# Kernel optimization log

Measured on AMD Instinct MI355X. Metric: run time of the kernel, lower is better.

The kernel has to match this reference:

```python
import jax, jax.numpy as jnp
import numpy as np

D_V, D_Q, D_H = 256, 128, 64

def setup_inputs() -> dict:
    key = jax.random.key(0)
    ks = jax.random.split(key, 8)
    B, T = 512, 512
    query = jax.random.normal(ks[0], (B, D_Q), dtype=jnp.float32)
    values = jax.random.normal(ks[1], (B, T, D_V), dtype=jnp.float32)
    s1 = 1.0 / np.sqrt(D_V)
    s2 = 1.0 / np.sqrt(D_Q)
    sv = 1.0 / np.sqrt(D_H)
    W1 = jax.random.uniform(ks[2], (D_H, D_V), jnp.float32, -s1, s1)
    b1 = jax.random.uniform(ks[3], (D_H,), jnp.float32, -s1, s1)
    W2 = jax.random.uniform(ks[4], (D_H, D_Q), jnp.float32, -s2, s2)
    b2 = jax.random.uniform(ks[5], (D_H,), jnp.float32, -s2, s2)
    Wv = jax.random.uniform(ks[6], (1, D_H), jnp.float32, -sv, sv)
    bv = jax.random.uniform(ks[7], (1,), jnp.float32, -sv, sv)
    return {"query": query, "values": values, "W1": W1, "b1": b1,
            "W2": W2, "b2": b2, "Wv": Wv, "bv": bv}

def reference(query, values, W1, b1, W2, b2, Wv, bv):
    # hidden_with_time_axis: [B,1,128]
    h = jnp.einsum('btv,hv->bth', values, W1) + b1 \
        + (jnp.einsum('bq,hq->bh', query, W2) + b2)[:, None, :]   # [B,T,64]
    score = jnp.einsum('bth,oh->bto', jnp.tanh(h), Wv) + bv        # [B,T,1]
    attention_weights = jax.nn.softmax(score, axis=0)              # softmax over dim 0, as written
    context_vector = jnp.sum(attention_weights * values, axis=0)   # [T,256]
    return (context_vector, attention_weights)
```

## Files before the change

kernel.cpp:

```cpp
#include <hip/hip_runtime.h>
#include <hip/hip_bf16.h>

#define Tt 512
#define Bb 512
#define DV 256
#define DQ 128
#define DH 64
#define CTXN (Tt * DV)
#define VBF_BYTES ((size_t)Bb * Tt * DV * 2)

typedef __attribute__((ext_vector_type(8))) short bf16x8;
typedef __attribute__((ext_vector_type(8))) unsigned short u16x8;
typedef __attribute__((ext_vector_type(4))) float f32x4;

__device__ __forceinline__ unsigned short f2bf(float x) {
  unsigned u = __float_as_uint(x);
  u += 0x7FFFu + ((u >> 16) & 1u);
  return (unsigned short)(u >> 16);
}
__device__ __forceinline__ float bf2f(unsigned short b) {
  return __uint_as_float(((unsigned)b) << 16);
}

__global__ void prep_kernel(const float* __restrict__ query,
                            const float* __restrict__ W1,
                            const float* __restrict__ W2,
                            const float* __restrict__ b1,
                            const float* __restrict__ b2,
                            float* __restrict__ qh,
                            unsigned short* __restrict__ w1bf) {
  __shared__ float q[DQ];
  const int blk = blockIdx.x;
  const int h = threadIdx.x;
  if (blk < Bb) {
    q[h]      = query[blk * DQ + h];
    q[h + 64] = query[blk * DQ + h + 64];
    __syncthreads();
    const float* w2r = W2 + h * DQ;
    float acc = 0.f;
#pragma unroll 8
    for (int k = 0; k < DQ; ++k) acc = fmaf(w2r[k], q[k], acc);
    qh[blk * DH + h] = acc + b1[h] + b2[h];
  } else {
    int base = (blk - Bb) * 256;
#pragma unroll
    for (int k = 0; k < 4; ++k) {
      int i = base + (k << 6) + h;
      w1bf[i] = f2bf(W1[i]);
    }
  }
}

template <bool WRITEV>
__global__ __launch_bounds__(256, 4) void score2_kernel(
    const float* __restrict__ values,
    const unsigned short* __restrict__ w1bf,
    const float* __restrict__ qh,
    const float* __restrict__ Wv,
    const float* __restrict__ bv,
    float* __restrict__ esT,
    unsigned short* __restrict__ vbf) {
  __shared__ __align__(16) unsigned short lB[DH * DV];
  const int tid = threadIdx.x;
  const int m0 = blockIdx.x * 64;
  const int bidx = m0 >> 9;

  const uint4* w1v = (const uint4*)w1bf;
#pragma unroll
  for (int i = 0; i < 8; ++i) {
    int vec = i * 256 + tid;
    uint4 d = w1v[vec];
    int row = vec >> 5;
    int u = vec & 31;
    int byte = (row << 9) + (u << 4);
    *(uint4*)((char*)lB + (byte ^ ((row & 7) << 4))) = d;
  }
  __syncthreads();

  const int wv = tid >> 6;
  const int lane = tid & 63;
  const int lrow = lane & 15;
  const int g = lane >> 4;

  f32x4 acc[4];
#pragma unroll
  for (int nt = 0; nt < 4; ++nt) acc[nt] = (f32x4){0.f, 0.f, 0.f, 0.f};

  const int arow = wv * 16 + lrow;
  const float* ap = values + (size_t)(m0 + arow) * DV;
  unsigned short* vst = WRITEV
      ? vbf + (size_t)(m0 + arow) * DV + g * 8
      : nullptr;

#pragma unroll
  for (int ks = 0; ks < 8; ++ks) {
    const float* fp = ap + ks * 32 + g * 8;
    float4 f0 = *(const float4*)(fp);
    float4 f1 = *(const float4*)(fp + 4);
    bf16x8 af;
    af[0] = (short)f2bf(f0.x); af[1] = (short)f2bf(f0.y);
    af[2] = (short)f2bf(f0.z); af[3] = (short)f2bf(f0.w);
    af[4] = (short)f2bf(f1.x); af[5] = (short)f2bf(f1.y);
    af[6] = (short)f2bf(f1.z); af[7] = (short)f2bf(f1.w);
    if (WRITEV) *(bf16x8*)(vst + ks * 32) = af;
    int k2 = (ks * 32 + g * 8) * 2;
#pragma unroll
    for (int nt = 0; nt < 4; ++nt) {
      int brow = nt * 16 + lrow;
      bf16x8 bf = *(const bf16x8*)((const char*)lB +
                                   (((brow << 9) + k2) ^ ((brow & 7) << 4)));
      acc[nt] = __builtin_amdgcn_mfma_f32_16x16x32_bf16(af, bf, acc[nt], 0, 0, 0);
    }
  }

  float bv0 = bv[0];
  float sc[4] = {0.f, 0.f, 0.f, 0.f};
#pragma unroll
  for (int nt = 0; nt < 4; ++nt) {
    int col = nt * 16 + lrow;
    float qv = qh[bidx * DH + col];
    float wvc = Wv[col];
#pragma unroll
    for (int j = 0; j < 4; ++j) {
      float hv = acc[nt][j] + qv;
      float e = __expf(2.f * hv);
      float th = (e - 1.f) / (e + 1.f);
      sc[j] = fmaf(th, wvc, sc[j]);
    }
  }
#pragma unroll
  for (int j = 0; j < 4; ++j) {
    float v = sc[j];
    v += __shfl_xor(v, 1);
    v += __shfl_xor(v, 2);
    v += __shfl_xor(v, 4);
    v += __shfl_xor(v, 8);
    sc[j] = v;
  }
  if (lrow == 0) {
#pragma unroll
    for (int j = 0; j < 4; ++j) {
      int m = m0 + wv * 16 + g * 4 + j;
      int tt = m & (Tt - 1);
      esT[tt * Bb + bidx] = __expf(sc[j] + bv0);
    }
  }
}

__global__ __launch_bounds__(1024, 2) void ctx2_kernel(
    const float* __restrict__ values,
    const unsigned short* __restrict__ vbf,
    const float* __restrict__ esT,
    int use_bf,
    float* __restrict__ out) {
  const int t = blockIdx.x;
  const int tid = threadIdx.x;
  const int wv = tid >> 6, lane = tid & 63;
  __shared__ float wbuf[Bb];
  __shared__ float ssum[16];
  __shared__ float red[32][DV];

  float es = (tid < Bb) ? esT[t * Bb + tid] : 0.f;
  float zs = es;
#pragma unroll
  for (int d = 1; d < 64; d <<= 1) zs += __shfl_xor(zs, d);
  if (lane == 0) ssum[wv] = zs;
  if (tid < Bb) wbuf[tid] = es;
  __syncthreads();
  float Z = 0.f;
#pragma unroll
  for (int i = 0; i < 16; ++i) Z += ssum[i];
  const float invZ = 1.f / Z;
  if (tid < Bb)
    out[CTXN + tid * Tt + t] = es * invZ;

  const int unit = tid & 31;
  const int brow = tid >> 5;
  float av[8] = {0.f, 0.f, 0.f, 0.f, 0.f, 0.f, 0.f, 0.f};
#pragma unroll 4
  for (int i = 0; i < 16; ++i) {
    int b = (i << 5) + brow;
    float w = wbuf[b];
    if (use_bf) {
      u16x8 v = *(const u16x8*)(vbf + ((size_t)b * Tt + t) * DV + unit * 8);
#pragma unroll
      for (int j = 0; j < 8; ++j) av[j] = fmaf(w, bf2f(v[j]), av[j]);
    } else {
      const float* p = values + ((size_t)b * Tt + t) * DV + unit * 8;
      float4 a = ((const float4*)p)[0];
      float4 c = ((const float4*)p)[1];
      av[0] = fmaf(w, a.x, av[0]); av[1] = fmaf(w, a.y, av[1]);
      av[2] = fmaf(w, a.z, av[2]); av[3] = fmaf(w, a.w, av[3]);
      av[4] = fmaf(w, c.x, av[4]); av[5] = fmaf(w, c.y, av[5]);
      av[6] = fmaf(w, c.z, av[6]); av[7] = fmaf(w, c.w, av[7]);
    }
  }
#pragma unroll
  for (int j = 0; j < 8; ++j) red[brow][unit * 8 + j] = av[j];
  __syncthreads();
  if (tid < DV) {
    float tot = 0.f;
#pragma unroll
    for (int b = 0; b < 32; ++b) tot += red[b][tid];
    out[t * DV + tid] = tot * invZ;
  }
}

extern "C" void kernel_launch(void* const* d_in, const int* in_sizes, int n_in,
                              void* d_out, int out_size, void* d_ws, size_t ws_size,
                              hipStream_t stream) {
  const float* query  = (const float*)d_in[0];
  const float* values = (const float*)d_in[1];
  const float* W1     = (const float*)d_in[2];
  const float* b1     = (const float*)d_in[3];
  const float* W2     = (const float*)d_in[4];
  const float* b2     = (const float*)d_in[5];
  const float* Wv     = (const float*)d_in[6];
  const float* bv     = (const float*)d_in[7];
  float* out = (float*)d_out;
  char* ws = (char*)d_ws;
  float* qh            = (float*)ws;
  unsigned short* w1bf = (unsigned short*)(ws + 131072);
  float* esT           = (float*)(ws + 163840);
  unsigned short* vbf  = (unsigned short*)(ws + (size_t)2 * 1024 * 1024);
  const bool use_bf = ws_size >= (size_t)2 * 1024 * 1024 + VBF_BYTES;

  prep_kernel<<<dim3(Bb + 64), dim3(64), 0, stream>>>(query, W1, W2, b1, b2, qh, w1bf);
  if (use_bf) {
    score2_kernel<true><<<dim3((Bb * Tt) / 64), dim3(256), 0, stream>>>(
        values, w1bf, qh, Wv, bv, esT, vbf);
    ctx2_kernel<<<dim3(Tt), dim3(1024), 0, stream>>>(values, vbf, esT, 1, out);
  } else {
    score2_kernel<false><<<dim3((Bb * Tt) / 64), dim3(256), 0, stream>>>(
        values, w1bf, qh, Wv, bv, esT, nullptr);
    ctx2_kernel<<<dim3(Tt), dim3(1024), 0, stream>>>(values, nullptr, esT, 0, out);
  }
}
```

Before: 111.7 us.

## Drop bf16 values copy, read fp32 values in ctx, reverse batch order

Removes the bf16 copy of values that the score kernel wrote and that the context kernel read. The context kernel now reads fp32 values directly and walks batches in reverse order, so the most recently streamed rows may still be in cache. The strided attention-weight output write moves into a new transpose kernel that uses a shared-memory tile and a per-t invZ buffer. This trades the 128MB bf16 write plus 128MB read for a 256MB fp32 reread of values, and adds one more launch.

```diff
diff --git a/kernel.cpp b/kernel.cpp
--- a/kernel.cpp
+++ b/kernel.cpp
@@ -7,19 +7,14 @@
 #define DQ 128
 #define DH 64
 #define CTXN (Tt * DV)
-#define VBF_BYTES ((size_t)Bb * Tt * DV * 2)
 
 typedef __attribute__((ext_vector_type(8))) short bf16x8;
-typedef __attribute__((ext_vector_type(8))) unsigned short u16x8;
 typedef __attribute__((ext_vector_type(4))) float f32x4;
 
 __device__ __forceinline__ unsigned short f2bf(float x) {
   unsigned u = __float_as_uint(x);
   u += 0x7FFFu + ((u >> 16) & 1u);
   return (unsigned short)(u >> 16);
-}
-__device__ __forceinline__ float bf2f(unsigned short b) {
-  return __uint_as_float(((unsigned)b) << 16);
 }
 
 __global__ void prep_kernel(const float* __restrict__ query,
@@ -51,15 +46,13 @@
   }
 }
 
-template <bool WRITEV>
-__global__ __launch_bounds__(256, 4) void score2_kernel(
+__global__ __launch_bounds__(256, 4) void score_kernel(
     const float* __restrict__ values,
     const unsigned short* __restrict__ w1bf,
     const float* __restrict__ qh,
     const float* __restrict__ Wv,
     const float* __restrict__ bv,
-    float* __restrict__ esT,
-    unsigned short* __restrict__ vbf) {
+    float* __restrict__ esT) {
   __shared__ __align__(16) unsigned short lB[DH * DV];
   const int tid = threadIdx.x;
   const int m0 = blockIdx.x * 64;
@@ -88,9 +81,6 @@
 
   const int arow = wv * 16 + lrow;
   const float* ap = values + (size_t)(m0 + arow) * DV;
-  unsigned short* vst = WRITEV
-      ? vbf + (size_t)(m0 + arow) * DV + g * 8
-      : nullptr;
 
 #pragma unroll
   for (int ks = 0; ks < 8; ++ks) {
@@ -102,7 +92,6 @@
     af[2] = (short)f2bf(f0.z); af[3] = (short)f2bf(f0.w);
     af[4] = (short)f2bf(f1.x); af[5] = (short)f2bf(f1.y);
     af[6] = (short)f2bf(f1.z); af[7] = (short)f2bf(f1.w);
-    if (WRITEV) *(bf16x8*)(vst + ks * 32) = af;
     int k2 = (ks * 32 + g * 8) * 2;
 #pragma unroll
     for (int nt = 0; nt < 4; ++nt) {
@@ -147,11 +136,10 @@
   }
 }
 
-__global__ __launch_bounds__(1024, 2) void ctx2_kernel(
+__global__ __launch_bounds__(1024, 2) void ctx3_kernel(
     const float* __restrict__ values,
-    const unsigned short* __restrict__ vbf,
     const float* __restrict__ esT,
-    int use_bf,
+    float* __restrict__ invZbuf,
     float* __restrict__ out) {
   const int t = blockIdx.x;
   const int tid = threadIdx.x;
@@ -171,38 +159,54 @@
 #pragma unroll
   for (int i = 0; i < 16; ++i) Z += ssum[i];
   const float invZ = 1.f / Z;
-  if (tid < Bb)
-    out[CTXN + tid * Tt + t] = es * invZ;
+  if (tid == 0) invZbuf[t] = invZ;
 
   const int unit = tid & 31;
-  const int brow = tid >> 5;
+  const int b0 = tid >> 5;
   float av[8] = {0.f, 0.f, 0.f, 0.f, 0.f, 0.f, 0.f, 0.f};
 #pragma unroll 4
   for (int i = 0; i < 16; ++i) {
-    int b = (i << 5) + brow;
+    int b = ((15 - i) << 5) + b0;
     float w = wbuf[b];
-    if (use_bf) {
-      u16x8 v = *(const u16x8*)(vbf + ((size_t)b * Tt + t) * DV + unit * 8);
-#pragma unroll
-      for (int j = 0; j < 8; ++j) av[j] = fmaf(w, bf2f(v[j]), av[j]);
-    } else {
-      const float* p = values + ((size_t)b * Tt + t) * DV + unit * 8;
-      float4 a = ((const float4*)p)[0];
-      float4 c = ((const float4*)p)[1];
-      av[0] = fmaf(w, a.x, av[0]); av[1] = fmaf(w, a.y, av[1]);
-      av[2] = fmaf(w, a.z, av[2]); av[3] = fmaf(w, a.w, av[3]);
-      av[4] = fmaf(w, c.x, av[4]); av[5] = fmaf(w, c.y, av[5]);
-      av[6] = fmaf(w, c.z, av[6]); av[7] = fmaf(w, c.w, av[7]);
-    }
-  }
-#pragma unroll
-  for (int j = 0; j < 8; ++j) red[brow][unit * 8 + j] = av[j];
+    const float* p = values + ((size_t)b * Tt + t) * DV + unit * 8;
+    float4 a = ((const float4*)p)[0];
+    float4 c = ((const float4*)p)[1];
+    av[0] = fmaf(w, a.x, av[0]); av[1] = fmaf(w, a.y, av[1]);
+    av[2] = fmaf(w, a.z, av[2]); av[3] = fmaf(w, a.w, av[3]);
+    av[4] = fmaf(w, c.x, av[4]); av[5] = fmaf(w, c.y, av[5]);
+    av[6] = fmaf(w, c.z, av[6]); av[7] = fmaf(w, c.w, av[7]);
+  }
+#pragma unroll
+  for (int j = 0; j < 8; ++j) red[b0][unit * 8 + j] = av[j];
   __syncthreads();
   if (tid < DV) {
     float tot = 0.f;
 #pragma unroll
     for (int b = 0; b < 32; ++b) tot += red[b][tid];
     out[t * DV + tid] = tot * invZ;
+  }
+}
+
+__global__ __launch_bounds__(256) void fin_w_kernel(
+    const float* __restrict__ esT, const float* __restrict__ invZbuf,
+    float* __restrict__ out) {
+  __shared__ float tile[64][65];
+  const int tid = threadIdx.x;
+  const int t0 = (blockIdx.x >> 3) * 64;
+  const int b0 = (blockIdx.x & 7) * 64;
+  const int rr = tid >> 6;
+  const int cc = tid & 63;
+#pragma unroll
+  for (int k = 0; k < 16; ++k) {
+    int r = rr + (k << 2);
+    tile[r][cc] = esT[(t0 + r) * Bb + b0 + cc];
+  }
+  const float iz = invZbuf[t0 + cc];
+  __syncthreads();
+#pragma unroll
+  for (int k = 0; k < 16; ++k) {
+    int br = rr + (k << 2);
+    out[CTXN + (size_t)(b0 + br) * Tt + t0 + cc] = tile[cc][br] * iz;
   }
 }
 
@@ -222,17 +226,11 @@
   float* qh            = (float*)ws;
   unsigned short* w1bf = (unsigned short*)(ws + 131072);
   float* esT           = (float*)(ws + 163840);
-  unsigned short* vbf  = (unsigned short*)(ws + (size_t)2 * 1024 * 1024);
-  const bool use_bf = ws_size >= (size_t)2 * 1024 * 1024 + VBF_BYTES;
+  float* invZbuf       = (float*)(ws + 1212416);
 
   prep_kernel<<<dim3(Bb + 64), dim3(64), 0, stream>>>(query, W1, W2, b1, b2, qh, w1bf);
-  if (use_bf) {
-    score2_kernel<true><<<dim3((Bb * Tt) / 64), dim3(256), 0, stream>>>(
-        values, w1bf, qh, Wv, bv, esT, vbf);
-    ctx2_kernel<<<dim3(Tt), dim3(1024), 0, stream>>>(values, vbf, esT, 1, out);
-  } else {
-    score2_kernel<false><<<dim3((Bb * Tt) / 64), dim3(256), 0, stream>>>(
-        values, w1bf, qh, Wv, bv, esT, nullptr);
-    ctx2_kernel<<<dim3(Tt), dim3(1024), 0, stream>>>(values, nullptr, esT, 0, out);
-  }
-}
+  score_kernel<<<dim3((Bb * Tt) / 64), dim3(256), 0, stream>>>(
+      values, w1bf, qh, Wv, bv, esT);
+  ctx3_kernel<<<dim3(Tt), dim3(1024), 0, stream>>>(values, esT, invZbuf, out);
+  fin_w_kernel<<<dim3(64), dim3(256), 0, stream>>>(esT, invZbuf, out);
+}
```

Result: faster. 95.47 us, median of 2 (-14.5%).
